# Performance work log

Hardware: AMD Instinct MI355X
Metric: run time of the kernel (lower is better)

The kernel has to match this reference:

```python
import jax, jax.numpy as jnp
import numpy as np


def setup_inputs() -> dict:
    key = jax.random.key(0)
    k1, k2 = jax.random.split(key)
    x = jax.random.normal(k1, (8, 32, 252, 252), dtype=jnp.float32)
    weight = jax.random.normal(k2, (32, 32, 5, 5), dtype=jnp.float32)
    return {"x": x, "weight": weight}


def reference(x, weight):
    # FFT-based conv2d, mathematically identical to the torch module but with
    # the batch-invariant weight FFT hoisted out of the batch dimension.
    k = weight.shape[-1]
    p = k // 2
    # reflect padding (matches F.pad mode='reflect')
    xp = jnp.pad(x, ((0, 0), (0, 0), (p, p), (p, p)), mode="reflect")
    H, W = xp.shape[-2], xp.shape[-1]
    # embed kernel in top-left of a full-size zero canvas, then circular roll
    # by (-k)//2 (Python floor division, as in the original torch code)
    wp = jnp.zeros((weight.shape[0], weight.shape[1], H, W), dtype=x.dtype)
    wp = wp.at[:, :, :k, :k].set(weight)
    shift = (-k) // 2  # e.g. k=5 -> -3, matching torch.roll(shifts=(-k//2,...))
    wp = jnp.roll(wp, shift=(shift, shift), axis=(-2, -1))
    x_fft = jnp.fft.fft2(xp)          # [B, I, H, W] complex
    w_fft = jnp.fft.fft2(wp)          # [O, I, H, W] complex (no batch copy)
    out_fft = jnp.einsum("bihw,oihw->bohw", x_fft, w_fft)
    out = jnp.fft.ifft2(out_fft).real
    return out[:, :, p:-p, p:-p]
```

## Files before the change

kernel.cpp:

```cpp
#include <hip/hip_runtime.h>
#include <hip/hip_bf16.h>

typedef __attribute__((ext_vector_type(8))) short bf16x8;
typedef __attribute__((ext_vector_type(4))) float f32x4;

#define HW_   252
#define PLANE 63504
#define NCH   32
#define WS_NEED (25600u * 2u)

__device__ __forceinline__ unsigned short f2bf(float f) {
    unsigned u = __builtin_bit_cast(unsigned, f);
    u += 0x7FFFu + ((u >> 16) & 1u);
    return (unsigned short)(u >> 16);
}

__device__ __forceinline__ int padmap(int p) {
    int t = (p & 255) - 2;
    t = t < 0 ? -t : t;
    return t > 251 ? 502 - t : t;
}

__global__ void pack_w_kernel(const float* __restrict__ w, unsigned short* __restrict__ wp) {
    int e = blockIdx.x * 256 + threadIdx.x;
    if (e >= 25600) return;
    int ci = e & 31;
    int o  = (e >> 5) & 31;
    int t  = e >> 10;
    int da = t / 5, db = t - da * 5;
    wp[e] = f2bf(w[((o * 32 + ci) * 5 + (4 - da)) * 5 + (4 - db)]);
}

__global__ __launch_bounds__(256, 4) void conv_fused_v2(
    const float* __restrict__ x,
    const unsigned short* __restrict__ wp,
    float* __restrict__ out)
{
    __shared__ unsigned short xl[32 * 20 * 32];

    const int tid  = threadIdx.x;
    const int orig = blockIdx.x;
    const int b    = orig & 7;
    const int idx  = orig >> 3;
    const int rt   = idx >> 4;
    const int ct   = idx & 15;
    const int i0 = rt * 28, j0 = ct * 16;

    float v[10][8];
    {
        const float* xb = x + (size_t)b * NCH * PLANE;
        #pragma unroll
        for (int it = 0; it < 10; ++it) {
            int task = it * 256 + tid;
            int g    = task & 3;
            int pc   = task >> 2;
            int pr   = pc / 20;
            int col  = pc - pr * 20;
            const float* src = xb + (size_t)(g * 8) * PLANE
                                  + (size_t)padmap(i0 + 1 + pr) * HW_
                                  + padmap(j0 + 1 + col);
            #pragma unroll
            for (int q = 0; q < 8; ++q)
                v[it][q] = src[q * PLANE];
        }
    }
    #pragma unroll
    for (int it = 0; it < 10; ++it) {
        int task = it * 256 + tid;
        unsigned short pk[8];
        #pragma unroll
        for (int q = 0; q < 8; ++q)
            pk[q] = __builtin_bit_cast(unsigned short,
                        __float2bfloat16(v[it][q]));
        *reinterpret_cast<uint4*>(reinterpret_cast<char*>(xl) + task * 16)
            = *reinterpret_cast<const uint4*>(pk);
    }
    __syncthreads();

    const int lane = tid & 63;
    const int wid  = tid >> 6;
    const int lm   = lane & 15;
    const int lg   = lane >> 4;
    const int rowb = wid * 7;

    const char* xlb = reinterpret_cast<const char*>(xl);
    const char* wb  = reinterpret_cast<const char*>(wp);
    const int afix  = (lm << 6) + (lg << 4);
    const int j     = j0 + lm;

    f32x4 acc[7][2];
    #pragma unroll
    for (int r = 0; r < 7; ++r) {
        acc[r][0] = (f32x4){0.f, 0.f, 0.f, 0.f};
        acc[r][1] = (f32x4){0.f, 0.f, 0.f, 0.f};
    }

    #pragma unroll
    for (int db = 0; db < 5; ++db) {
        bf16x8 a[5][2];
        #pragma unroll
        for (int da = 0; da < 5; ++da) {
            const char* ap = wb + ((da * 5 + db) << 11) + afix;
            a[da][0] = *reinterpret_cast<const bf16x8*>(ap);
            a[da][1] = *reinterpret_cast<const bf16x8*>(ap + 1024);
        }

        #pragma unroll
        for (int l = 0; l < 11; ++l) {
            bf16x8 bf = *reinterpret_cast<const bf16x8*>(
                xlb + (rowb + l) * 1280 + ((lm + db) << 6) + (lg << 4));
            #pragma unroll
            for (int da = 0; da < 5; ++da) {
                const int r = l - da;
                if (r >= 0 && r < 7) {
                    acc[r][0] = __builtin_amdgcn_mfma_f32_16x16x32_bf16(
                        a[da][0], bf, acc[r][0], 0, 0, 0);
                    acc[r][1] = __builtin_amdgcn_mfma_f32_16x16x32_bf16(
                        a[da][1], bf, acc[r][1], 0, 0, 0);
                }
            }
        }
    }

    #pragma unroll
    for (int r = 0; r < 7; ++r) {
        const int i = i0 + rowb + r;
        if (j < HW_) {
            #pragma unroll
            for (int mt = 0; mt < 2; ++mt) {
                size_t rowoff = ((size_t)(b * NCH + mt * 16 + lg * 4)) * PLANE
                              + (size_t)i * HW_ + j;
                #pragma unroll
                for (int q = 0; q < 4; ++q)
                    out[rowoff + (size_t)q * PLANE] = acc[r][mt][q];
            }
        }
    }
}

__global__ __launch_bounds__(256) void conv_mfma_fb(
    const float* __restrict__ x,
    const float* __restrict__ w_raw,
    float* __restrict__ out)
{
    __shared__ unsigned short xl[12800];
    __shared__ unsigned short wl[25600];
    __shared__ int rmap[20], cmap[20];

    const int tid = threadIdx.x;
    const int bid = blockIdx.x;
    const int b  = bid >> 8;
    const int rt = (bid >> 4) & 15;
    const int ct = bid & 15;
    const int i0 = rt * 16, j0 = ct * 16;

    if (tid < 40) {
        int k    = tid < 20 ? tid : tid - 20;
        int base = tid < 20 ? i0  : j0;
        int r = (base + 1 + k) & 255;
        int t = r - 2;
        int m = t < 0 ? -t : (t > 251 ? 502 - t : t);
        if (tid < 20) rmap[k] = m; else cmap[k] = m;
    }
    for (int e = tid; e < 25600; e += 256) {
        int o   = e / 800;
        int rem = e - o * 800;
        int ci  = rem / 25;
        int kd  = rem - ci * 25;
        wl[(24 - kd) * 1024 + o * 32 + ci] = f2bf(w_raw[e]);
    }
    __syncthreads();

    for (int task = tid; task < 1600; task += 256) {
        int col = task % 20;
        int g   = (task / 20) & 3;
        int row = task / 80;
        const float* src = x + (size_t)(b * NCH + g * 8) * PLANE
                             + (size_t)rmap[row] * HW_ + cmap[col];
        unsigned short pk[8];
        #pragma unroll
        for (int q = 0; q < 8; ++q) pk[q] = f2bf(src[q * PLANE]);
        int off = ((row * 20 + col) << 6) + ((g ^ (col & 3)) << 4);
        *reinterpret_cast<uint4*>(reinterpret_cast<char*>(xl) + off)
            = *reinterpret_cast<const uint4*>(pk);
    }
    __syncthreads();

    const int lane  = tid & 63;
    const int wid   = tid >> 6;
    const int lm    = lane & 15;
    const int lg    = lane >> 4;
    const int rbase = wid * 4;

    f32x4 acc[4][2];
    #pragma unroll
    for (int rr = 0; rr < 4; ++rr) {
        acc[rr][0] = (f32x4){0.f, 0.f, 0.f, 0.f};
        acc[rr][1] = (f32x4){0.f, 0.f, 0.f, 0.f};
    }

    const char* wbase = (const char*)wl;
    const int afix = (lm << 6) + (lg << 4);
    const char* xlb = reinterpret_cast<const char*>(xl);

    #pragma unroll
    for (int da = 0; da < 5; ++da) {
        #pragma unroll
        for (int db = 0; db < 5; ++db) {
            const int t = da * 5 + db;
            bf16x8 a0 = *reinterpret_cast<const bf16x8*>(wbase + (t << 11) + afix);
            bf16x8 a1 = *reinterpret_cast<const bf16x8*>(wbase + (t << 11) + 1024 + afix);
            const int col  = lm + db;
            const int coff = (col << 6) + ((lg ^ (col & 3)) << 4);
            #pragma unroll
            for (int rr = 0; rr < 4; ++rr) {
                const int row = rbase + rr + da;
                bf16x8 bf = *reinterpret_cast<const bf16x8*>(xlb + row * 1280 + coff);
                acc[rr][0] = __builtin_amdgcn_mfma_f32_16x16x32_bf16(a0, bf, acc[rr][0], 0, 0, 0);
                acc[rr][1] = __builtin_amdgcn_mfma_f32_16x16x32_bf16(a1, bf, acc[rr][1], 0, 0, 0);
            }
        }
    }

    const int j = j0 + lm;
    #pragma unroll
    for (int rr = 0; rr < 4; ++rr) {
        const int i = i0 + rbase + rr;
        if (i < HW_ && j < HW_) {
            size_t rowoff = (size_t)(b * NCH) * PLANE + (size_t)i * HW_ + j;
            #pragma unroll
            for (int mt = 0; mt < 2; ++mt)
                #pragma unroll
                for (int q = 0; q < 4; ++q) {
                    int o = mt * 16 + lg * 4 + q;
                    out[rowoff + (size_t)o * PLANE] = acc[rr][mt][q];
                }
        }
    }
}

extern "C" void kernel_launch(void* const* d_in, const int* in_sizes, int n_in,
                              void* d_out, int out_size, void* d_ws, size_t ws_size,
                              hipStream_t stream) {
    const float* x = (const float*)d_in[0];
    const float* w = (const float*)d_in[1];
    float* out = (float*)d_out;

    if (ws_size >= WS_NEED) {
        unsigned short* wp = (unsigned short*)d_ws;
        hipLaunchKernelGGL(pack_w_kernel, dim3(100), dim3(256), 0, stream, w, wp);
        hipLaunchKernelGGL(conv_fused_v2, dim3(1152), dim3(256), 0, stream,
                           x, (const unsigned short*)wp, out);
    } else {
        hipLaunchKernelGGL(conv_mfma_fb, dim3(2048), dim3(256), 0, stream, x, w, out);
    }
}
```

Measured before the change: 46.72 us.

## Shrink conv row tile to 16 and vectorize padded input staging loads

Reduces the per-block output tile from 28 to 16 rows (4 rows per wave), which gives 2048 blocks instead of 1152, a smaller LDS buffer and raises the occupancy hint to 5. The input halo staging now has each thread load 4 contiguous columns with float4 reads for interior columns, falling back to scalar reflect-mapped reads only near the edges. The aim is better occupancy and coalescing in exchange for a larger halo overhead (more redundant input rows and weight reloads per output).

```diff
diff --git a/kernel.cpp b/kernel.cpp
--- a/kernel.cpp
+++ b/kernel.cpp
@@ -31,12 +31,12 @@
     wp[e] = f2bf(w[((o * 32 + ci) * 5 + (4 - da)) * 5 + (4 - db)]);
 }
 
-__global__ __launch_bounds__(256, 4) void conv_fused_v2(
+__global__ __launch_bounds__(256, 5) void conv_fused_v3(
     const float* __restrict__ x,
     const unsigned short* __restrict__ wp,
     float* __restrict__ out)
 {
-    __shared__ unsigned short xl[32 * 20 * 32];
+    __shared__ unsigned short xl[20 * 20 * 32];
 
     const int tid  = threadIdx.x;
     const int orig = blockIdx.x;
@@ -44,36 +44,51 @@
     const int idx  = orig >> 3;
     const int rt   = idx >> 4;
     const int ct   = idx & 15;
-    const int i0 = rt * 28, j0 = ct * 16;
-
-    float v[10][8];
+    const int i0 = rt * 16, j0 = ct * 16;
+
     {
         const float* xb = x + (size_t)b * NCH * PLANE;
         #pragma unroll
-        for (int it = 0; it < 10; ++it) {
+        for (int it = 0; it < 2; ++it) {
             int task = it * 256 + tid;
-            int g    = task & 3;
-            int pc   = task >> 2;
-            int pr   = pc / 20;
-            int col  = pc - pr * 20;
-            const float* src = xb + (size_t)(g * 8) * PLANE
-                                  + (size_t)padmap(i0 + 1 + pr) * HW_
-                                  + padmap(j0 + 1 + col);
-            #pragma unroll
-            for (int q = 0; q < 8; ++q)
-                v[it][q] = src[q * PLANE];
-        }
-    }
-    #pragma unroll
-    for (int it = 0; it < 10; ++it) {
-        int task = it * 256 + tid;
-        unsigned short pk[8];
-        #pragma unroll
-        for (int q = 0; q < 8; ++q)
-            pk[q] = __builtin_bit_cast(unsigned short,
-                        __float2bfloat16(v[it][q]));
-        *reinterpret_cast<uint4*>(reinterpret_cast<char*>(xl) + task * 16)
-            = *reinterpret_cast<const uint4*>(pk);
+            if (task < 400) {
+                int g  = task & 3;
+                int pc = task >> 2;
+                int pr = pc / 5;
+                int c4 = pc - pr * 5;
+                const float* rowp = xb + (size_t)(g * 8) * PLANE
+                                       + (size_t)padmap(i0 + 1 + pr) * HW_;
+                const int p0 = j0 + 1 + c4 * 4;
+                float v[8][4];
+                if (p0 >= 2 && p0 <= 250) {
+                    const float* src = rowp + (p0 - 2);
+                    #pragma unroll
+                    for (int q = 0; q < 8; ++q)
+                        *reinterpret_cast<float4*>(v[q]) =
+                            *reinterpret_cast<const float4*>(src + (size_t)q * PLANE);
+                } else {
+                    int mc[4];
+                    #pragma unroll
+                    for (int k = 0; k < 4; ++k) mc[k] = padmap(p0 + k);
+                    #pragma unroll
+                    for (int q = 0; q < 8; ++q)
+                        #pragma unroll
+                        for (int k = 0; k < 4; ++k)
+                            v[q][k] = rowp[(size_t)q * PLANE + mc[k]];
+                }
+                char* lbase = reinterpret_cast<char*>(xl) + ((pc * 4) << 6) + (g << 4);
+                #pragma unroll
+                for (int k = 0; k < 4; ++k) {
+                    unsigned short pk[8];
+                    #pragma unroll
+                    for (int q = 0; q < 8; ++q)
+                        pk[q] = __builtin_bit_cast(unsigned short,
+                                    __float2bfloat16(v[q][k]));
+                    *reinterpret_cast<uint4*>(lbase + (k << 6)) =
+                        *reinterpret_cast<const uint4*>(pk);
+                }
+            }
+        }
     }
     __syncthreads();
 
@@ -81,16 +96,16 @@
     const int wid  = tid >> 6;
     const int lm   = lane & 15;
     const int lg   = lane >> 4;
-    const int rowb = wid * 7;
+    const int rowb = wid * 4;
 
     const char* xlb = reinterpret_cast<const char*>(xl);
     const char* wb  = reinterpret_cast<const char*>(wp);
     const int afix  = (lm << 6) + (lg << 4);
     const int j     = j0 + lm;
 
-    f32x4 acc[7][2];
-    #pragma unroll
-    for (int r = 0; r < 7; ++r) {
+    f32x4 acc[4][2];
+    #pragma unroll
+    for (int r = 0; r < 4; ++r) {
         acc[r][0] = (f32x4){0.f, 0.f, 0.f, 0.f};
         acc[r][1] = (f32x4){0.f, 0.f, 0.f, 0.f};
     }
@@ -106,13 +121,13 @@
         }
 
         #pragma unroll
-        for (int l = 0; l < 11; ++l) {
+        for (int l = 0; l < 8; ++l) {
             bf16x8 bf = *reinterpret_cast<const bf16x8*>(
                 xlb + (rowb + l) * 1280 + ((lm + db) << 6) + (lg << 4));
             #pragma unroll
             for (int da = 0; da < 5; ++da) {
                 const int r = l - da;
-                if (r >= 0 && r < 7) {
+                if (r >= 0 && r < 4) {
                     acc[r][0] = __builtin_amdgcn_mfma_f32_16x16x32_bf16(
                         a[da][0], bf, acc[r][0], 0, 0, 0);
                     acc[r][1] = __builtin_amdgcn_mfma_f32_16x16x32_bf16(
@@ -123,9 +138,9 @@
     }
 
     #pragma unroll
-    for (int r = 0; r < 7; ++r) {
+    for (int r = 0; r < 4; ++r) {
         const int i = i0 + rowb + r;
-        if (j < HW_) {
+        if (i < HW_ && j < HW_) {
             #pragma unroll
             for (int mt = 0; mt < 2; ++mt) {
                 size_t rowoff = ((size_t)(b * NCH + mt * 16 + lg * 4)) * PLANE
@@ -249,7 +264,7 @@
     if (ws_size >= WS_NEED) {
         unsigned short* wp = (unsigned short*)d_ws;
         hipLaunchKernelGGL(pack_w_kernel, dim3(100), dim3(256), 0, stream, w, wp);
-        hipLaunchKernelGGL(conv_fused_v2, dim3(1152), dim3(256), 0, stream,
+        hipLaunchKernelGGL(conv_fused_v3, dim3(2048), dim3(256), 0, stream,
                            x, (const unsigned short*)wp, out);
     } else {
         hipLaunchKernelGGL(conv_mfma_fb, dim3(2048), dim3(256), 0, stream, x, w, out);
```

Measured after the change: 57.97 us. +24.1%, slower.

## Vectorize input staging with float4 loads and swap MFMA operands for float4 stores

Applied to the files above, without the earlier changes.

The input tile is now staged with float4 row loads on 16-byte-aligned column quads, using a wider 24-column LDS row. A scalar reflect-padding path handles edge quads. The MFMA A/B operands are swapped so each lane holds four consecutive output columns, which allows float4 global stores in place of scalar strided stores. Launch bounds drop from 4 to 3 blocks per SM and LDS use grows, which can reduce occupancy. The goal is to cut the number of global memory transactions on both the load and store sides.

```diff
diff --git a/kernel.cpp b/kernel.cpp
--- a/kernel.cpp
+++ b/kernel.cpp
@@ -1,5 +1,4 @@
 #include <hip/hip_runtime.h>
-#include <hip/hip_bf16.h>
 
 typedef __attribute__((ext_vector_type(8))) short bf16x8;
 typedef __attribute__((ext_vector_type(4))) float f32x4;
@@ -31,12 +30,12 @@
     wp[e] = f2bf(w[((o * 32 + ci) * 5 + (4 - da)) * 5 + (4 - db)]);
 }
 
-__global__ __launch_bounds__(256, 4) void conv_fused_v2(
+__global__ __launch_bounds__(256, 3) void conv_fused_v4(
     const float* __restrict__ x,
     const unsigned short* __restrict__ wp,
     float* __restrict__ out)
 {
-    __shared__ unsigned short xl[32 * 20 * 32];
+    __shared__ unsigned short xl[32 * 24 * 32];
 
     const int tid  = threadIdx.x;
     const int orig = blockIdx.x;
@@ -46,34 +45,46 @@
     const int ct   = idx & 15;
     const int i0 = rt * 28, j0 = ct * 16;
 
-    float v[10][8];
     {
         const float* xb = x + (size_t)b * NCH * PLANE;
         #pragma unroll
-        for (int it = 0; it < 10; ++it) {
+        for (int it = 0; it < 3; ++it) {
             int task = it * 256 + tid;
-            int g    = task & 3;
-            int pc   = task >> 2;
-            int pr   = pc / 20;
-            int col  = pc - pr * 20;
-            const float* src = xb + (size_t)(g * 8) * PLANE
-                                  + (size_t)padmap(i0 + 1 + pr) * HW_
-                                  + padmap(j0 + 1 + col);
-            #pragma unroll
-            for (int q = 0; q < 8; ++q)
-                v[it][q] = src[q * PLANE];
-        }
-    }
-    #pragma unroll
-    for (int it = 0; it < 10; ++it) {
-        int task = it * 256 + tid;
-        unsigned short pk[8];
-        #pragma unroll
-        for (int q = 0; q < 8; ++q)
-            pk[q] = __builtin_bit_cast(unsigned short,
-                        __float2bfloat16(v[it][q]));
-        *reinterpret_cast<uint4*>(reinterpret_cast<char*>(xl) + task * 16)
-            = *reinterpret_cast<const uint4*>(pk);
+            int quad = task % 6;
+            int pg   = task / 6;
+            int pr   = pg >> 2;
+            int g    = pg & 3;
+            int row  = padmap(i0 + 1 + pr);
+            int s0   = j0 - 4 + quad * 4;
+            const float* rowp = xb + (size_t)(g * 8) * PLANE + (size_t)row * HW_;
+            float vv[8][4];
+            if (s0 >= 0 && s0 + 3 <= 251) {
+                const float* src = rowp + s0;
+                #pragma unroll
+                for (int q = 0; q < 8; ++q)
+                    *reinterpret_cast<float4*>(vv[q]) =
+                        *reinterpret_cast<const float4*>(src + (size_t)q * PLANE);
+            } else {
+                int mc[4];
+                #pragma unroll
+                for (int k = 0; k < 4; ++k) mc[k] = padmap(s0 + k + 2);
+                #pragma unroll
+                for (int q = 0; q < 8; ++q)
+                    #pragma unroll
+                    for (int k = 0; k < 4; ++k)
+                        vv[q][k] = rowp[(size_t)q * PLANE + mc[k]];
+            }
+            char* lbase = reinterpret_cast<char*>(xl)
+                        + ((pr * 24 + quad * 4) << 6) + (g << 4);
+            #pragma unroll
+            for (int k = 0; k < 4; ++k) {
+                unsigned short pk[8];
+                #pragma unroll
+                for (int q = 0; q < 8; ++q) pk[q] = f2bf(vv[q][k]);
+                *reinterpret_cast<uint4*>(lbase + (k << 6)) =
+                    *reinterpret_cast<const uint4*>(pk);
+            }
+        }
     }
     __syncthreads();
 
@@ -86,7 +97,6 @@
     const char* xlb = reinterpret_cast<const char*>(xl);
     const char* wb  = reinterpret_cast<const char*>(wp);
     const int afix  = (lm << 6) + (lg << 4);
-    const int j     = j0 + lm;
 
     f32x4 acc[7][2];
     #pragma unroll
@@ -108,31 +118,30 @@
         #pragma unroll
         for (int l = 0; l < 11; ++l) {
             bf16x8 bf = *reinterpret_cast<const bf16x8*>(
-                xlb + (rowb + l) * 1280 + ((lm + db) << 6) + (lg << 4));
+                xlb + (rowb + l) * 1536 + ((lm + db + 3) << 6) + (lg << 4));
             #pragma unroll
             for (int da = 0; da < 5; ++da) {
                 const int r = l - da;
                 if (r >= 0 && r < 7) {
                     acc[r][0] = __builtin_amdgcn_mfma_f32_16x16x32_bf16(
-                        a[da][0], bf, acc[r][0], 0, 0, 0);
+                        bf, a[da][0], acc[r][0], 0, 0, 0);
                     acc[r][1] = __builtin_amdgcn_mfma_f32_16x16x32_bf16(
-                        a[da][1], bf, acc[r][1], 0, 0, 0);
+                        bf, a[da][1], acc[r][1], 0, 0, 0);
                 }
             }
         }
     }
 
-    #pragma unroll
-    for (int r = 0; r < 7; ++r) {
-        const int i = i0 + rowb + r;
-        if (j < HW_) {
+    if (j0 + (lg << 2) < HW_) {
+        #pragma unroll
+        for (int r = 0; r < 7; ++r) {
+            const int i = i0 + rowb + r;
             #pragma unroll
             for (int mt = 0; mt < 2; ++mt) {
-                size_t rowoff = ((size_t)(b * NCH + mt * 16 + lg * 4)) * PLANE
-                              + (size_t)i * HW_ + j;
-                #pragma unroll
-                for (int q = 0; q < 4; ++q)
-                    out[rowoff + (size_t)q * PLANE] = acc[r][mt][q];
+                float* dst = out + ((size_t)(b * NCH + mt * 16 + lm)) * PLANE
+                           + (size_t)i * HW_ + j0 + (lg << 2);
+                *reinterpret_cast<float4*>(dst) =
+                    *reinterpret_cast<const float4*>(&acc[r][mt]);
             }
         }
     }
@@ -249,7 +258,7 @@
     if (ws_size >= WS_NEED) {
         unsigned short* wp = (unsigned short*)d_ws;
         hipLaunchKernelGGL(pack_w_kernel, dim3(100), dim3(256), 0, stream, w, wp);
-        hipLaunchKernelGGL(conv_fused_v2, dim3(1152), dim3(256), 0, stream,
+        hipLaunchKernelGGL(conv_fused_v4, dim3(1152), dim3(256), 0, stream,
                            x, (const unsigned short*)wp, out);
     } else {
         hipLaunchKernelGGL(conv_mfma_fb, dim3(2048), dim3(256), 0, stream, x, w, out);
```

Result: slower. 66.36 us (+42.0%).
